# Kernel tuning notes

Measured on AMD Instinct MI355X. Metric: run time of the kernel, lower is better.

The kernel has to match this reference:

```python
import jax, jax.numpy as jnp
import numpy as np

KERNEL = 3
PAD = KERNEL // 2  # 1


def cal_wfft_ortho(weight, n, cout, cin):
    # weight: [N, M, k, k] with M < N
    nf = n // 2 + 1
    vfft = jnp.fft.rfft2(weight, s=(n, n), norm='ortho')          # [N, M, n, nf] complex
    vfft = jnp.transpose(vfft, (2, 3, 0, 1))                       # [n, nf, N, M]
    vH = jnp.conj(jnp.swapaxes(vfft, -1, -2))                      # [n, nf, M, N]
    wfft = vH @ vfft                                               # [n, nf, M, M] Gram
    perturb_ratio = 1e-5
    eps = jnp.mean(jnp.diagonal(wfft, axis1=-2, axis2=-1), axis=-1) * perturb_ratio
    m = wfft.shape[-1]
    wfft = wfft + eps[..., None, None] * jnp.eye(m, dtype=wfft.dtype)
    N = vfft.shape[-2]
    I = jnp.eye(N, dtype=wfft.dtype)
    # Cayley-style orthogonal projector: I - 2 V (V^H V)^{-1} V^H
    ortho = I - 2.0 * (vfft @ jnp.linalg.solve(wfft, vH))          # [n, nf, N, N]
    ortho = ortho[:, :, :cout, :cin]
    return ortho.reshape(n * nf, cout, cin)


def setup_inputs() -> dict:
    key = jax.random.key(0)
    k1, k2, k3 = jax.random.split(key, 3)
    B, C, H = 64, 256, 32
    x = jax.random.normal(k1, (B, C, H, H), dtype=jnp.float32)
    # masked low-rank orthogonal weight: [cout, cin-1, 3, 3]
    weight = jax.random.normal(k2, (C, C - 1, KERNEL, KERNEL), dtype=jnp.float32) * 0.05
    bias = jax.random.normal(k3, (C,), dtype=jnp.float32) * 0.01
    return {"x": x, "weight": weight, "bias": bias}


def reference(x, weight, bias):
    B, cin, h, _ = x.shape
    cout = weight.shape[0]
    xp = jnp.pad(x, ((0, 0), (0, 0), (PAD, PAD), (PAD, PAD)))
    n = h + 2 * PAD
    nf = n // 2 + 1
    # x to frequency domain: [n*nf, cin, B]
    xfft = jnp.fft.rfft2(xp, norm='ortho')                         # [B, cin, n, nf]
    xfft = jnp.transpose(xfft, (2, 3, 1, 0)).reshape(n * nf, cin, B)
    W = cal_wfft_ortho(weight, n, cout, cin)                       # [n*nf, cout, cin]
    zfft = W @ xfft                                                # [n*nf, cout, B]
    zfft = jnp.transpose(zfft.reshape(n, nf, cout, B), (3, 2, 0, 1))
    z = jnp.fft.irfft2(zfft, norm='ortho')                         # [B, cout, n, n] real
    z = z[:, :, PAD:-PAD, PAD:-PAD]
    z = z + bias[:, None, None]
    return z
```

## Files before the change

kernel.cpp:

```cpp
#include <hip/hip_runtime.h>
#include <math.h>

#define NN    34
#define NFH   18
#define NFREQ 612
#define CH    256
#define CIN   255
#define NB    64
#define HW    32
#define PI2   6.2831853071795864769f
#define TSTRIDE 36864

__device__ __forceinline__ int tIdx(int I, int J){ return ((I*(I+1))>>1) + J; }

__global__ __launch_bounds__(256) void kF1(const float* __restrict__ x, float2* __restrict__ U){
  __shared__ float tc[NFH][HW], ts[NFH][HW];
  int tid = threadIdx.x;
  for (int i = tid; i < NFH*HW; i += 256){
    int kx = i >> 5, w = i & 31;
    float s, c; sincosf(-PI2*(float)(kx*(w+1))/34.f, &s, &c);
    tc[kx][w] = c; ts[kx][w] = s;
  }
  __syncthreads();
  int c = blockIdx.x;
  int a = (blockIdx.y << 2) + (tid >> 6);
  int b = tid & 63;
  const float4* xr = (const float4*)(x + (((size_t)b*CH + c)*HW + a)*HW);
  float xv[HW];
#pragma unroll
  for (int t = 0; t < 8; t++){
    float4 v = xr[t];
    xv[4*t] = v.x; xv[4*t+1] = v.y; xv[4*t+2] = v.z; xv[4*t+3] = v.w;
  }
#pragma unroll 1
  for (int kx = 0; kx < NFH; kx++){
    float re = 0.f, im = 0.f;
#pragma unroll
    for (int w = 0; w < HW; w++){ re += xv[w]*tc[kx][w]; im += xv[w]*ts[kx][w]; }
    U[(((size_t)a*NFH + kx)*CH + c)*NB + b] = make_float2(re, im);
  }
}

__global__ __launch_bounds__(512) void kF2(const float2* __restrict__ U, float2* __restrict__ X){
  __shared__ float pc[NN][HW], ps[NN][HW];
  int tid = threadIdx.x;
  for (int i = tid; i < NN*HW; i += 512){
    int ky = i >> 5, a = i & 31;
    float s, c; sincosf(-PI2*(float)(ky*(a+1))/34.f, &s, &c);
    pc[ky][a] = c*(1.f/34.f); ps[ky][a] = s*(1.f/34.f);
  }
  __syncthreads();
  int kx = blockIdx.x;
  int c  = (blockIdx.y << 3) + (tid >> 6);
  int b  = tid & 63;
  float2 u[HW];
#pragma unroll
  for (int a = 0; a < HW; a++) u[a] = U[(((size_t)a*NFH + kx)*CH + c)*NB + b];
#pragma unroll 1
  for (int ky = 0; ky < NN; ky++){
    float re = 0.f, im = 0.f;
#pragma unroll
    for (int a = 0; a < HW; a++){
      float cc = pc[ky][a], ss = ps[ky][a];
      re += u[a].x*cc - u[a].y*ss;
      im += u[a].x*ss + u[a].y*cc;
    }
    X[(((size_t)ky*NFH + kx)*CH + c)*NB + b] = make_float2(re, im);
  }
}

__global__ __launch_bounds__(256) void kT0(const float* __restrict__ w, float* __restrict__ wT){
  int idx = blockIdx.x*256 + threadIdx.x;
  if (idx >= 9*CH*CIN) return;
  int k = idx / (CH*CIN);
  int r = idx - k*(CH*CIN);
  wT[idx] = w[(size_t)r*9 + k];
}

__global__ __launch_bounds__(256) void kC(const float* __restrict__ wT, float* __restrict__ C2){
  int kk = blockIdx.x;
  int k1 = kk / 9, k2 = kk - k1*9;
  int to = (blockIdx.y >> 2) << 6, tp = (blockIdx.y & 3) << 6;
  __shared__ float As[64][33], Bs[64][33];
  int tid = threadIdx.x;
  int ty = tid >> 4, tx = tid & 15;
  float acc[4][4] = {};
  const float* Ab = wT + (size_t)k1*CH*CIN;
  const float* Bb = wT + (size_t)k2*CH*CIN;
  for (int i0 = 0; i0 < CIN; i0 += 32){
    for (int idx = tid; idx < 64*32; idx += 256){
      int r = idx >> 5, j = idx & 31;
      int i = i0 + j;
      As[r][j] = (i < CIN) ? Ab[(size_t)(to + r)*CIN + i] : 0.f;
      Bs[r][j] = (i < CIN) ? Bb[(size_t)(tp + r)*CIN + i] : 0.f;
    }
    __syncthreads();
#pragma unroll
    for (int j = 0; j < 32; j++){
      float av[4], bv[4];
#pragma unroll
      for (int d = 0; d < 4; d++){ av[d] = As[ty*4+d][j]; bv[d] = Bs[tx*4+d][j]; }
#pragma unroll
      for (int da = 0; da < 4; da++)
#pragma unroll
        for (int db = 0; db < 4; db++) acc[da][db] += av[da]*bv[db];
    }
    __syncthreads();
  }
  float* Cb = C2 + (size_t)kk*CH*CH;
#pragma unroll
  for (int da = 0; da < 4; da++)
#pragma unroll
    for (int db = 0; db < 4; db++)
      Cb[(size_t)(to + ty*4 + da)*CH + tp + tx*4 + db] = acc[da][db];
}

__global__ __launch_bounds__(64) void kM(const float* __restrict__ C2, float2* __restrict__ M, int cf0, int cF){
  int t = blockIdx.x;
  int I = 0;
  while ((((I+1)*(I+2))>>1) <= t) I++;
  int J = t - ((I*(I+1))>>1);
  int r = blockIdx.y;
  int o = I*32 + r, p0 = J*32;
  int fl = (blockIdx.z << 6) + threadIdx.x;
  bool act = fl < cF;
  int f = act ? (cf0 + fl) : 0;
  int ky = f / NFH, kx = f - ky*NFH;
  float Pc[5], Ps[5], Qc[5], Qs[5];
#pragma unroll
  for (int d = 0; d < 5; d++){
    float s, c;
    sincosf(-PI2*(float)(ky*(d-2))/34.f, &s, &c);
    Pc[d] = c*(1.f/1156.f); Ps[d] = s*(1.f/1156.f);
    sincosf(-PI2*(float)(kx*(d-2))/34.f, &s, &c);
    Qc[d] = c; Qs[d] = s;
  }
  float ax[32] = {}, ay[32] = {};
  const float* Cb = C2 + (size_t)o*CH + p0;
#pragma unroll 1
  for (int k1 = 0; k1 < 9; k1++){
#pragma unroll 1
    for (int k2 = 0; k2 < 9; k2++){
      int da = k1/3 - k2/3 + 2, db = k1%3 - k2%3 + 2;
      float cr = Pc[da]*Qc[db] - Ps[da]*Qs[db];
      float ci = Pc[da]*Qs[db] + Ps[da]*Qc[db];
      const float* crow = Cb + (size_t)(k1*9 + k2)*CH*CH;
#pragma unroll
      for (int j = 0; j < 32; j++){
        float cv = crow[j];
        ax[j] += cv*cr; ay[j] += cv*ci;
      }
    }
  }
  if (act){
    float2* Mr = M + (size_t)fl*TSTRIDE + ((size_t)t << 10) + (r << 5);
#pragma unroll
    for (int j = 0; j < 32; j++) Mr[j] = make_float2(ax[j], ay[j]);
  }
}

__global__ __launch_bounds__(256) void kEps(float2* __restrict__ M, float* __restrict__ eb, int cf0){
  int fi = blockIdx.x;
  int o = threadIdx.x;
  int I = o >> 5, r = o & 31;
  float2* Mf = M + (size_t)fi*TSTRIDE + ((size_t)tIdx(I,I) << 10) + r*32 + r;
  __shared__ float red[256];
  float d = Mf->x;
  red[o] = d;
  __syncthreads();
  for (int s = 128; s > 0; s >>= 1){ if (o < s) red[o] += red[o+s]; __syncthreads(); }
  float eps = red[0] * (1e-5f/255.f);
  Mf->x = d + eps;
  if (o == 0) eb[cf0 + fi] = eps;
}

__global__ __launch_bounds__(256) void kPanel(float2* __restrict__ Mg, int pb){
  __shared__ float2 colbuf[2][32];
  __shared__ float darr[32];
  int fi = blockIdx.x;
  float2* Tf = Mg + (size_t)fi*TSTRIDE;
  const int h = CH - (pb << 5);
  const int i = threadIdx.x;
  const bool act = i < h;
  float2* rowp = Tf + ((size_t)tIdx(pb + (i >> 5), pb) << 10) + ((i & 31) << 5);
  float2 r[32];
  if (act){
#pragma unroll
    for (int t = 0; t < 16; t++){
      float4 v = ((const float4*)rowp)[t];
      r[2*t]   = make_float2(v.x, v.y);
      r[2*t+1] = make_float2(v.z, v.w);
    }
  }
#pragma unroll
  for (int k = 0; k < 32; k++){
    if (act && i >= k && i < 32) colbuf[k & 1][i] = r[k];
    __syncthreads();
    float pinv = __builtin_amdgcn_rcpf(colbuf[k & 1][k].x);
    if (act && i > k){
      float ax = r[k].x * pinv, ay = r[k].y * pinv;
#pragma unroll
      for (int j = k + 1; j < 32; j++){
        float2 l = colbuf[k & 1][j];
        r[j].x -= ax*l.x + ay*l.y;
        r[j].y -= ay*l.x - ax*l.y;
      }
    }
  }
  if (act && i < 32) darr[i] = r[i].x;
  __syncthreads();
  if (act){
#pragma unroll
    for (int j = 0; j < 32; j++){
      float sc = __frsqrt_rn(fmaxf(darr[j], 1e-30f));
      r[j].x *= sc; r[j].y *= sc;
    }
#pragma unroll
    for (int t = 0; t < 16; t++)
      ((float4*)rowp)[t] = make_float4(r[2*t].x, r[2*t].y, r[2*t+1].x, r[2*t+1].y);
  }
}

__global__ __launch_bounds__(256) void kSyrk(float2* __restrict__ Mg, int pb){
  __shared__ float2 As[32][33], Bs[32][33];
  int fi = blockIdx.x;
  int p = blockIdx.y;
  int li = 0;
  while ((((li+1)*(li+2)) >> 1) <= p) li++;
  int lj = p - ((li*(li+1)) >> 1);
  int I = pb + 1 + li, J = pb + 1 + lj;
  float2* Tf = Mg + (size_t)fi*TSTRIDE;
  const float2* Asrc = Tf + ((size_t)tIdx(I, pb) << 10);
  const float2* Bsrc = Tf + ((size_t)tIdx(J, pb) << 10);
  float2* Cdst = Tf + ((size_t)tIdx(I, J) << 10);
  int tid = threadIdx.x;
  for (int idx = tid; idx < 1024; idx += 256){
    int r = idx >> 5, c = idx & 31;
    As[r][c] = Asrc[idx];
    Bs[r][c] = Bsrc[idx];
  }
  int r = tid >> 3, c0 = (tid & 7) << 2;
  float2 acc[4];
  float4 c01 = *(const float4*)(Cdst + r*32 + c0);
  float4 c23 = *(const float4*)(Cdst + r*32 + c0 + 2);
  acc[0] = make_float2(c01.x, c01.y); acc[1] = make_float2(c01.z, c01.w);
  acc[2] = make_float2(c23.x, c23.y); acc[3] = make_float2(c23.z, c23.w);
  __syncthreads();
#pragma unroll 4
  for (int k = 0; k < 32; k++){
    float2 a = As[r][k];
#pragma unroll
    for (int d = 0; d < 4; d++){
      float2 b = Bs[c0 + d][k];
      acc[d].x -= a.x*b.x + a.y*b.y;
      acc[d].y -= a.y*b.x - a.x*b.y;
    }
  }
  *(float4*)(Cdst + r*32 + c0)     = make_float4(acc[0].x, acc[0].y, acc[1].x, acc[1].y);
  *(float4*)(Cdst + r*32 + c0 + 2) = make_float4(acc[2].x, acc[2].y, acc[3].x, acc[3].y);
}


template<int RB>
__device__ __forceinline__ void updF(float2 (&s)[8][4], const float2* __restrict__ tb,
                                     const float2* __restrict__ vb, int r, int hf){
#pragma unroll 2
  for (int k = 0; k < 32; k++){
    float2 l = tb[r*33 + k];
    const float2* vp = vb + k*10 + (hf<<2);
    float2 v0 = vp[0], v1 = vp[1], v2 = vp[2], v3 = vp[3];
    s[RB][0].x -= l.x*v0.x - l.y*v0.y; s[RB][0].y -= l.x*v0.y + l.y*v0.x;
    s[RB][1].x -= l.x*v1.x - l.y*v1.y; s[RB][1].y -= l.x*v1.y + l.y*v1.x;
    s[RB][2].x -= l.x*v2.x - l.y*v2.y; s[RB][2].y -= l.x*v2.y + l.y*v2.x;
    s[RB][3].x -= l.x*v3.x - l.y*v3.y; s[RB][3].y -= l.x*v3.y + l.y*v3.x;
  }
}

template<int RB>
__device__ __forceinline__ void updB(float2 (&s)[8][4], const float2* __restrict__ tb,
                                     const float2* __restrict__ vb, int r, int hf){
#pragma unroll 2
  for (int k = 0; k < 32; k++){
    float2 l = tb[k*33 + r];
    const float2* vp = vb + k*10 + (hf<<2);
    float2 v0 = vp[0], v1 = vp[1], v2 = vp[2], v3 = vp[3];
    s[RB][0].x -= l.x*v0.x + l.y*v0.y; s[RB][0].y -= l.x*v0.y - l.y*v0.x;
    s[RB][1].x -= l.x*v1.x + l.y*v1.y; s[RB][1].y -= l.x*v1.y - l.y*v1.x;
    s[RB][2].x -= l.x*v2.x + l.y*v2.y; s[RB][2].y -= l.x*v2.y - l.y*v2.x;
    s[RB][3].x -= l.x*v3.x + l.y*v3.y; s[RB][3].y -= l.x*v3.y - l.y*v3.x;
  }
}

template<int JB>
__device__ __forceinline__ void diagF(float2 (&s)[8][4], const float2* __restrict__ tb,
                                      float2* __restrict__ vb, int r, int hf){
  float2 sv0 = s[JB][0], sv1 = s[JB][1], sv2 = s[JB][2], sv3 = s[JB][3];
  int src = hf << 5;
#pragma unroll 1
  for (int k = 0; k < 32; k++){
    float dinv = __builtin_amdgcn_rcpf(tb[k*33 + k].x);
    float c0x = sv0.x*dinv, c0y = sv0.y*dinv;
    float c1x = sv1.x*dinv, c1y = sv1.y*dinv;
    float c2x = sv2.x*dinv, c2y = sv2.y*dinv;
    float c3x = sv3.x*dinv, c3y = sv3.y*dinv;
    float2 v0, v1, v2, v3;
    v0.x = __shfl(c0x, src + k, 64); v0.y = __shfl(c0y, src + k, 64);
    v1.x = __shfl(c1x, src + k, 64); v1.y = __shfl(c1y, src + k, 64);
    v2.x = __shfl(c2x, src + k, 64); v2.y = __shfl(c2y, src + k, 64);
    v3.x = __shfl(c3x, src + k, 64); v3.y = __shfl(c3y, src + k, 64);
    if (r == k){ sv0 = v0; sv1 = v1; sv2 = v2; sv3 = v3; }
    else if (r > k){
      float2 l = tb[r*33 + k];
      sv0.x -= l.x*v0.x - l.y*v0.y; sv0.y -= l.x*v0.y + l.y*v0.x;
      sv1.x -= l.x*v1.x - l.y*v1.y; sv1.y -= l.x*v1.y + l.y*v1.x;
      sv2.x -= l.x*v2.x - l.y*v2.y; sv2.y -= l.x*v2.y + l.y*v2.x;
      sv3.x -= l.x*v3.x - l.y*v3.y; sv3.y -= l.x*v3.y + l.y*v3.x;
    }
  }
  s[JB][0] = sv0; s[JB][1] = sv1; s[JB][2] = sv2; s[JB][3] = sv3;
  float2* wp = vb + r*10 + (hf<<2);
  wp[0] = sv0; wp[1] = sv1; wp[2] = sv2; wp[3] = sv3;
}

template<int JB>
__device__ __forceinline__ void diagB(float2 (&s)[8][4], const float2* __restrict__ tb,
                                      float2* __restrict__ vb, int r, int hf){
  float2 sv0 = s[JB][0], sv1 = s[JB][1], sv2 = s[JB][2], sv3 = s[JB][3];
  int src = hf << 5;
#pragma unroll 1
  for (int k = 31; k >= 0; k--){
    float dinv = __builtin_amdgcn_rcpf(tb[k*33 + k].x);
    float c0x = sv0.x*dinv, c0y = sv0.y*dinv;
    float c1x = sv1.x*dinv, c1y = sv1.y*dinv;
    float c2x = sv2.x*dinv, c2y = sv2.y*dinv;
    float c3x = sv3.x*dinv, c3y = sv3.y*dinv;
    float2 v0, v1, v2, v3;
    v0.x = __shfl(c0x, src + k, 64); v0.y = __shfl(c0y, src + k, 64);
    v1.x = __shfl(c1x, src + k, 64); v1.y = __shfl(c1y, src + k, 64);
    v2.x = __shfl(c2x, src + k, 64); v2.y = __shfl(c2y, src + k, 64);
    v3.x = __shfl(c3x, src + k, 64); v3.y = __shfl(c3y, src + k, 64);
    if (r == k){ sv0 = v0; sv1 = v1; sv2 = v2; sv3 = v3; }
    else if (r < k){
      float2 l = tb[k*33 + r];
      sv0.x -= l.x*v0.x + l.y*v0.y; sv0.y -= l.x*v0.y - l.y*v0.x;
      sv1.x -= l.x*v1.x + l.y*v1.y; sv1.y -= l.x*v1.y - l.y*v1.x;
      sv2.x -= l.x*v2.x + l.y*v2.y; sv2.y -= l.x*v2.y - l.y*v2.x;
      sv3.x -= l.x*v3.x + l.y*v3.y; sv3.y -= l.x*v3.y - l.y*v3.x;
    }
  }
  s[JB][0] = sv0; s[JB][1] = sv1; s[JB][2] = sv2; s[JB][3] = sv3;
  float2* wp = vb + r*10 + (hf<<2);
  wp[0] = sv0; wp[1] = sv1; wp[2] = sv2; wp[3] = sv3;
}

#define DISPATCH8(FN, V) \
  switch (V){ \
    case 0: FN<0>(s, tb, vb, r, hf); break; \
    case 1: FN<1>(s, tb, vb, r, hf); break; \
    case 2: FN<2>(s, tb, vb, r, hf); break; \
    case 3: FN<3>(s, tb, vb, r, hf); break; \
    case 4: FN<4>(s, tb, vb, r, hf); break; \
    case 5: FN<5>(s, tb, vb, r, hf); break; \
    case 6: FN<6>(s, tb, vb, r, hf); break; \
    default: FN<7>(s, tb, vb, r, hf); break; }

__global__ __launch_bounds__(128) void kSolve(const float2* __restrict__ Lg, float2* __restrict__ X,
                                              const float* __restrict__ eb, int cf0){
  __shared__ float2 tb2[2][32*33];
  __shared__ float2 vbuf[2][32*10];
  __shared__ int seq[72];
  int fi = blockIdx.x;
  int f = cf0 + fi;
  const float2* Tf = Lg + (size_t)fi*TSTRIDE;
  float2* Xf = X + (size_t)f*CH*NB;
  int tid = threadIdx.x, wv = tid >> 6, lane = tid & 63, hf = lane >> 5, r = lane & 31;
  int cc = (blockIdx.y << 4) + (wv << 3) + (hf << 2);
  if (tid == 0){
    int n = 0;
    for (int jb = 0; jb < 8; jb++){
      seq[n++] = jb | (jb << 4) | (1 << 12);
      for (int ib = jb+1; ib < 8; ib++) seq[n++] = ib | (jb << 4) | (0 << 12);
    }
    for (int jb = 7; jb >= 0; jb--){
      seq[n++] = jb | (jb << 4) | (2 << 12);
      for (int ii = jb-1; ii >= 0; ii--) seq[n++] = jb | (ii << 4) | (3 << 12);
    }
  }
  float2 s[8][4];
#pragma unroll
  for (int rb = 0; rb < 8; rb++){
    const float2* xp = Xf + (size_t)((rb << 5) + r)*NB + cc;
    float4 a = *(const float4*)xp, b = *(const float4*)(xp + 2);
    s[rb][0] = make_float2(a.x, a.y); s[rb][1] = make_float2(a.z, a.w);
    s[rb][2] = make_float2(b.x, b.y); s[rb][3] = make_float2(b.z, b.w);
  }
  {
    const float4* src = (const float4*)(Tf + (tid << 3));
    float4 a0 = src[0], a1 = src[1], a2 = src[2], a3 = src[3];
    int row = tid >> 2, col = (tid & 3) << 3;
    float2* d = &tb2[0][row*33 + col];
    d[0] = make_float2(a0.x, a0.y); d[1] = make_float2(a0.z, a0.w);
    d[2] = make_float2(a1.x, a1.y); d[3] = make_float2(a1.z, a1.w);
    d[4] = make_float2(a2.x, a2.y); d[5] = make_float2(a2.z, a2.w);
    d[6] = make_float2(a3.x, a3.y); d[7] = make_float2(a3.z, a3.w);
  }
  __syncthreads();
  float2* vb = vbuf[wv];
  int cur = 0;
#pragma unroll 1
  for (int t = 0; t < 72; t++){
    float4 p0, p1, p2, p3;
    bool pf = t < 71;
    if (pf){
      int e2 = seq[t+1];
      const float4* src = (const float4*)(Tf + ((size_t)tIdx(e2 & 15, (e2 >> 4) & 15) << 10) + (tid << 3));
      p0 = src[0]; p1 = src[1]; p2 = src[2]; p3 = src[3];
    }
    int e = seq[t];
    int type = e >> 12;
    const float2* tb = tb2[cur];
    if (type == 0){        int rbT = e & 15;        DISPATCH8(updF, rbT); }
    else if (type == 1){   int jb  = e & 15;        DISPATCH8(diagF, jb); }
    else if (type == 2){   int jb  = e & 15;        DISPATCH8(diagB, jb); }
    else {                 int rbT = (e >> 4) & 15; DISPATCH8(updB, rbT); }
    if (pf){
      int row = tid >> 2, col = (tid & 3) << 3;
      float2* d = &tb2[cur ^ 1][row*33 + col];
      d[0] = make_float2(p0.x, p0.y); d[1] = make_float2(p0.z, p0.w);
      d[2] = make_float2(p1.x, p1.y); d[3] = make_float2(p1.z, p1.w);
      d[4] = make_float2(p2.x, p2.y); d[5] = make_float2(p2.z, p2.w);
      d[6] = make_float2(p3.x, p3.y); d[7] = make_float2(p3.z, p3.w);
    }
    __syncthreads();
    cur ^= 1;
  }
  float te = 2.f * eb[f];
#pragma unroll
  for (int rb = 0; rb < 8; rb++){
    float2* xp = Xf + (size_t)((rb << 5) + r)*NB + cc;
    float4 a = *(const float4*)xp, b = *(const float4*)(xp + 2);
    *(float4*)xp       = make_float4(te*s[rb][0].x - a.x, te*s[rb][0].y - a.y,
                                     te*s[rb][1].x - a.z, te*s[rb][1].y - a.w);
    *(float4*)(xp + 2) = make_float4(te*s[rb][2].x - b.x, te*s[rb][2].y - b.y,
                                     te*s[rb][3].x - b.z, te*s[rb][3].y - b.w);
  }
}

__global__ __launch_bounds__(512) void kI1(const float2* __restrict__ X, float2* __restrict__ Y){
  __shared__ float pc[HW][NN], ps[HW][NN];
  int tid = threadIdx.x;
  for (int i = tid; i < HW*NN; i += 512){
    int a = i / NN, ky = i - a*NN;
    float s, c; sincosf(PI2*(float)(ky*(a+1))/34.f, &s, &c);
    pc[a][ky] = c; ps[a][ky] = s;
  }
  __syncthreads();
  int kx = blockIdx.x;
  int cc = (blockIdx.y << 3) + (tid >> 6);
  int b = tid & 63;
  float2 z[NN];
#pragma unroll
  for (int ky = 0; ky < NN; ky++) z[ky] = X[(((size_t)ky*NFH + kx)*CH + cc)*NB + b];
#pragma unroll 1
  for (int a = 0; a < HW; a++){
    float re = 0.f, im = 0.f;
#pragma unroll
    for (int ky = 0; ky < NN; ky++){
      float co = pc[a][ky], si = ps[a][ky];
      re += z[ky].x*co - z[ky].y*si;
      im += z[ky].x*si + z[ky].y*co;
    }
    Y[(((size_t)a*NFH + kx)*CH + cc)*NB + b] = make_float2(re, im);
  }
}

__global__ __launch_bounds__(256) void kI2(const float2* __restrict__ Y, const float* __restrict__ bias,
                                           float* __restrict__ out){
  __shared__ float tc[NFH][HW], tsn[NFH][HW];
  int tid = threadIdx.x;
  for (int i = tid; i < NFH*HW; i += 256){
    int kx = i >> 5, w = i & 31;
    float wt = (kx == 0 || kx == 17) ? (1.f/34.f) : (2.f/34.f);
    float s, c; sincosf(PI2*(float)(kx*(w+1))/34.f, &s, &c);
    tc[kx][w] = wt*c; tsn[kx][w] = wt*s;
  }
  __syncthreads();
  int cc = blockIdx.x;
  int a = (blockIdx.y << 2) + (tid >> 6);
  int b = tid & 63;
  float2 yv[NFH];
#pragma unroll
  for (int kx = 0; kx < NFH; kx++) yv[kx] = Y[(((size_t)a*NFH + kx)*CH + cc)*NB + b];
  float bi = bias[cc];
  float ov[HW];
#pragma unroll
  for (int w = 0; w < HW; w++){
    float acc = bi;
#pragma unroll
    for (int kx = 0; kx < NFH; kx++)
      acc += yv[kx].x*tc[kx][w] - yv[kx].y*tsn[kx][w];
    ov[w] = acc;
  }
  float4* op = (float4*)(out + (((size_t)b*CH + cc)*HW + a)*HW);
#pragma unroll
  for (int t = 0; t < 8; t++) op[t] = make_float4(ov[4*t], ov[4*t+1], ov[4*t+2], ov[4*t+3]);
}

extern "C" void kernel_launch(void* const* d_in, const int* in_sizes, int n_in,
                              void* d_out, int out_size, void* d_ws, size_t ws_size,
                              hipStream_t stream){
  (void)in_sizes; (void)n_in; (void)out_size;
  const float* x    = (const float*)d_in[0];
  const float* w    = (const float*)d_in[1];
  const float* bias = (const float*)d_in[2];
  float* out = (float*)d_out;
  char* ws = (char*)d_ws;

  const size_t X_BYTES  = (size_t)NFREQ*CH*NB*sizeof(float2);
  const size_t WT_BYTES = (size_t)9*CH*CIN*sizeof(float);
  const size_t C_BYTES  = (size_t)81*CH*CH*sizeof(float);
  const size_t offX  = 0;
  const size_t offWT = offX + X_BYTES;
  const size_t offC  = offWT + WT_BYTES;
  const size_t offE  = offC + C_BYTES;
  const size_t offChunk = offE + 4096;
  const size_t perF = (size_t)TSTRIDE * sizeof(float2);

  float2* X  = (float2*)(ws + offX);
  float*  wT = (float*)(ws + offWT);
  float*  C2 = (float*)(ws + offC);
  float*  eb = (float*)(ws + offE);
  float2* U  = (float2*)(ws + offChunk);
  float2* Mb = (float2*)(ws + offChunk);
  float2* Y  = (float2*)(ws + offChunk);

  size_t avail = ws_size > offChunk ? ws_size - offChunk : 0;
  int F = (int)(avail / perF);
  if (F < 1) F = 1;
  if (F > NFREQ) F = NFREQ;
  int nch = (NFREQ + F - 1) / F;
  F = (NFREQ + nch - 1) / nch;

  kF1<<<dim3(CH, 8), 256, 0, stream>>>(x, U);
  kF2<<<dim3(NFH, 32), 512, 0, stream>>>(U, X);
  kT0<<<(9*CH*CIN + 255)/256, 256, 0, stream>>>(w, wT);
  kC<<<dim3(81, 16), 256, 0, stream>>>(wT, C2);

  for (int cf0 = 0; cf0 < NFREQ; cf0 += F){
    int cF = (NFREQ - cf0 < F) ? (NFREQ - cf0) : F;
    kM<<<dim3(36, 32, (cF + 63) >> 6), 64, 0, stream>>>(C2, Mb, cf0, cF);
    kEps<<<cF, 256, 0, stream>>>(Mb, eb, cf0);
    for (int pb = 0; pb < 8; pb++){
      kPanel<<<cF, 256, 0, stream>>>(Mb, pb);
      int nrem = 7 - pb;
      int npairs = (nrem*(nrem+1)) >> 1;
      if (npairs > 0)
        kSyrk<<<dim3(cF, npairs), 256, 0, stream>>>(Mb, pb);
    }
    kSolve<<<dim3(cF, 4), 128, 0, stream>>>(Mb, X, eb, cf0);
  }

  kI1<<<dim3(NFH, 32), 512, 0, stream>>>(X, Y);
  kI2<<<dim3(CH, 8), 256, 0, stream>>>(Y, bias, out);
}
```

Before: 3.431 ms.

## Switch Cholesky to left-looking panel updates, dropping separate SYRK launches

Replaces the right-looking blocked Cholesky, with one panel kernel plus one trailing SYRK kernel per block step, by a left-looking variant. Each panel kernel now applies all earlier panel updates itself, streaming prior L tiles through shared memory before factoring. This removes the SYRK launches and repeated read/write of the trailing matrix, but every panel step now does serial work inside one block per frequency. Separately, the solve kernel's vector buffer pitch is changed from 10 to 9 and its grid is padded to a multiple of 8 with a bounds check.

```diff
diff --git a/kernel.cpp b/kernel.cpp
--- a/kernel.cpp
+++ b/kernel.cpp
@@ -174,7 +174,8 @@
   if (o == 0) eb[cf0 + fi] = eps;
 }
 
-__global__ __launch_bounds__(256) void kPanel(float2* __restrict__ Mg, int pb){
+__global__ __launch_bounds__(256) void kPanelL(float2* __restrict__ Mg, int pb){
+  __shared__ float2 Ls[32][33];
   __shared__ float2 colbuf[2][32];
   __shared__ float darr[32];
   int fi = blockIdx.x;
@@ -192,6 +193,39 @@
       r[2*t+1] = make_float2(v.z, v.w);
     }
   }
+#pragma unroll 1
+  for (int q = 0; q < pb; q++){
+    __syncthreads();
+    {
+      const float2* ts2 = Tf + ((size_t)tIdx(pb, q) << 10);
+      for (int idx = i; idx < 1024; idx += 256)
+        Ls[idx >> 5][idx & 31] = ts2[idx];
+    }
+    __syncthreads();
+    if (act){
+      const float4* lqp = (const float4*)(Tf + ((size_t)tIdx(pb + (i >> 5), q) << 10) + ((i & 31) << 5));
+#pragma unroll 1
+      for (int c4 = 0; c4 < 4; c4++){
+        float2 lq[8];
+#pragma unroll
+        for (int t = 0; t < 4; t++){
+          float4 v = lqp[c4*4 + t];
+          lq[2*t]   = make_float2(v.x, v.y);
+          lq[2*t+1] = make_float2(v.z, v.w);
+        }
+#pragma unroll 4
+        for (int j = 0; j < 32; j++){
+#pragma unroll
+          for (int k = 0; k < 8; k++){
+            float2 L = Ls[j][c4*8 + k];
+            r[j].x -= lq[k].x*L.x + lq[k].y*L.y;
+            r[j].y -= lq[k].y*L.x - lq[k].x*L.y;
+          }
+        }
+      }
+    }
+  }
+  __syncthreads();
 #pragma unroll
   for (int k = 0; k < 32; k++){
     if (act && i >= k && i < 32) colbuf[k & 1][i] = r[k];
@@ -221,45 +255,6 @@
   }
 }
 
-__global__ __launch_bounds__(256) void kSyrk(float2* __restrict__ Mg, int pb){
-  __shared__ float2 As[32][33], Bs[32][33];
-  int fi = blockIdx.x;
-  int p = blockIdx.y;
-  int li = 0;
-  while ((((li+1)*(li+2)) >> 1) <= p) li++;
-  int lj = p - ((li*(li+1)) >> 1);
-  int I = pb + 1 + li, J = pb + 1 + lj;
-  float2* Tf = Mg + (size_t)fi*TSTRIDE;
-  const float2* Asrc = Tf + ((size_t)tIdx(I, pb) << 10);
-  const float2* Bsrc = Tf + ((size_t)tIdx(J, pb) << 10);
-  float2* Cdst = Tf + ((size_t)tIdx(I, J) << 10);
-  int tid = threadIdx.x;
-  for (int idx = tid; idx < 1024; idx += 256){
-    int r = idx >> 5, c = idx & 31;
-    As[r][c] = Asrc[idx];
-    Bs[r][c] = Bsrc[idx];
-  }
-  int r = tid >> 3, c0 = (tid & 7) << 2;
-  float2 acc[4];
-  float4 c01 = *(const float4*)(Cdst + r*32 + c0);
-  float4 c23 = *(const float4*)(Cdst + r*32 + c0 + 2);
-  acc[0] = make_float2(c01.x, c01.y); acc[1] = make_float2(c01.z, c01.w);
-  acc[2] = make_float2(c23.x, c23.y); acc[3] = make_float2(c23.z, c23.w);
-  __syncthreads();
-#pragma unroll 4
-  for (int k = 0; k < 32; k++){
-    float2 a = As[r][k];
-#pragma unroll
-    for (int d = 0; d < 4; d++){
-      float2 b = Bs[c0 + d][k];
-      acc[d].x -= a.x*b.x + a.y*b.y;
-      acc[d].y -= a.y*b.x - a.x*b.y;
-    }
-  }
-  *(float4*)(Cdst + r*32 + c0)     = make_float4(acc[0].x, acc[0].y, acc[1].x, acc[1].y);
-  *(float4*)(Cdst + r*32 + c0 + 2) = make_float4(acc[2].x, acc[2].y, acc[3].x, acc[3].y);
-}
-
 
 template<int RB>
 __device__ __forceinline__ void updF(float2 (&s)[8][4], const float2* __restrict__ tb,
@@ -267,7 +262,7 @@
 #pragma unroll 2
   for (int k = 0; k < 32; k++){
     float2 l = tb[r*33 + k];
-    const float2* vp = vb + k*10 + (hf<<2);
+    const float2* vp = vb + k*9 + (hf<<2);
     float2 v0 = vp[0], v1 = vp[1], v2 = vp[2], v3 = vp[3];
     s[RB][0].x -= l.x*v0.x - l.y*v0.y; s[RB][0].y -= l.x*v0.y + l.y*v0.x;
     s[RB][1].x -= l.x*v1.x - l.y*v1.y; s[RB][1].y -= l.x*v1.y + l.y*v1.x;
@@ -282,7 +277,7 @@
 #pragma unroll 2
   for (int k = 0; k < 32; k++){
     float2 l = tb[k*33 + r];
-    const float2* vp = vb + k*10 + (hf<<2);
+    const float2* vp = vb + k*9 + (hf<<2);
     float2 v0 = vp[0], v1 = vp[1], v2 = vp[2], v3 = vp[3];
     s[RB][0].x -= l.x*v0.x + l.y*v0.y; s[RB][0].y -= l.x*v0.y - l.y*v0.x;
     s[RB][1].x -= l.x*v1.x + l.y*v1.y; s[RB][1].y -= l.x*v1.y - l.y*v1.x;
@@ -318,7 +313,7 @@
     }
   }
   s[JB][0] = sv0; s[JB][1] = sv1; s[JB][2] = sv2; s[JB][3] = sv3;
-  float2* wp = vb + r*10 + (hf<<2);
+  float2* wp = vb + r*9 + (hf<<2);
   wp[0] = sv0; wp[1] = sv1; wp[2] = sv2; wp[3] = sv3;
 }
 
@@ -349,7 +344,7 @@
     }
   }
   s[JB][0] = sv0; s[JB][1] = sv1; s[JB][2] = sv2; s[JB][3] = sv3;
-  float2* wp = vb + r*10 + (hf<<2);
+  float2* wp = vb + r*9 + (hf<<2);
   wp[0] = sv0; wp[1] = sv1; wp[2] = sv2; wp[3] = sv3;
 }
 
@@ -365,11 +360,12 @@
     default: FN<7>(s, tb, vb, r, hf); break; }
 
 __global__ __launch_bounds__(128) void kSolve(const float2* __restrict__ Lg, float2* __restrict__ X,
-                                              const float* __restrict__ eb, int cf0){
+                                              const float* __restrict__ eb, int cf0, int cF){
   __shared__ float2 tb2[2][32*33];
-  __shared__ float2 vbuf[2][32*10];
+  __shared__ float2 vbuf[2][32*9];
   __shared__ int seq[72];
   int fi = blockIdx.x;
+  if (fi >= cF) return;
   int f = cf0 + fi;
   const float2* Tf = Lg + (size_t)fi*TSTRIDE;
   float2* Xf = X + (size_t)f*CH*NB;
@@ -550,14 +546,10 @@
     int cF = (NFREQ - cf0 < F) ? (NFREQ - cf0) : F;
     kM<<<dim3(36, 32, (cF + 63) >> 6), 64, 0, stream>>>(C2, Mb, cf0, cF);
     kEps<<<cF, 256, 0, stream>>>(Mb, eb, cf0);
-    for (int pb = 0; pb < 8; pb++){
-      kPanel<<<cF, 256, 0, stream>>>(Mb, pb);
-      int nrem = 7 - pb;
-      int npairs = (nrem*(nrem+1)) >> 1;
-      if (npairs > 0)
-        kSyrk<<<dim3(cF, npairs), 256, 0, stream>>>(Mb, pb);
-    }
-    kSolve<<<dim3(cF, 4), 128, 0, stream>>>(Mb, X, eb, cf0);
+    for (int pb = 0; pb < 8; pb++)
+      kPanelL<<<cF, 256, 0, stream>>>(Mb, pb);
+    int cF8 = (cF + 7) & ~7;
+    kSolve<<<dim3(cF8, 4), 128, 0, stream>>>(Mb, X, eb, cf0, cF);
   }
 
   kI1<<<dim3(NFH, 32), 512, 0, stream>>>(X, Y);
```

Result: slower. 4.811 ms (+40.2%).
